# Performance work log

Measured on AMD Instinct MI355X. Metric: run time of the kernel, lower is better.

The kernel has to match this reference:

```python
import jax, jax.numpy as jnp
import numpy as np

N_NODES = 50000
N_EDGES = 800000
IN_DIM = 128
HIDDEN = 128


def setup_inputs() -> dict:
    key = jax.random.key(0)
    ks = jax.random.split(key, 6)
    x = jax.random.normal(ks[0], (N_NODES, IN_DIM), dtype=jnp.float32)
    edge_index = jax.random.randint(ks[1], (2, N_EDGES), 0, N_NODES, dtype=jnp.int32)
    W1 = jax.random.normal(ks[2], (IN_DIM, HIDDEN), dtype=jnp.float32) * 0.05
    b1 = jnp.zeros((HIDDEN,), dtype=jnp.float32)
    W2 = jax.random.normal(ks[3], (HIDDEN, HIDDEN), dtype=jnp.float32) * 0.05
    b2 = jnp.zeros((HIDDEN,), dtype=jnp.float32)
    return {"x": x, "edge_index": edge_index, "W1": W1, "b1": b1, "W2": W2, "b2": b2}


def _gcn_conv(x, W, b, src, dst, norm, n):
    # PyG GCNConv: linear transform, then normalized sum-aggregate, then bias.
    h = x @ W                                  # [N, H]
    msg = h[src] * norm[:, None]               # gather + scale  [E+N, H]
    out = jax.ops.segment_sum(msg, dst, num_segments=n)
    return out + b


def reference(x, edge_index, W1, b1, W2, b2):
    n = x.shape[0]
    # add self-loops (GCNConv default add_self_loops=True)
    loops = jnp.arange(n, dtype=edge_index.dtype)
    src = jnp.concatenate([edge_index[0], loops])
    dst = jnp.concatenate([edge_index[1], loops])
    # symmetric normalization: deg over destination nodes (edge_weight = 1)
    deg = jax.ops.segment_sum(jnp.ones(src.shape, dtype=x.dtype), dst, num_segments=n)
    dinv = jax.lax.rsqrt(deg)                  # deg >= 1 because of self-loops
    norm = dinv[src] * dinv[dst]               # [E+N]
    h = jax.nn.relu(_gcn_conv(x, W1, b1, src, dst, norm, n))
    return _gcn_conv(h, W2, b2, src, dst, norm, n)
```

## Files before the change

kernel.cpp:

```cpp
#include <hip/hip_runtime.h>

#define N_NODES 50000
#define N_EDGES 800000
#define DIM 128
#define CHUNK 4096
#define GRID 196
#define SEG_CAP 6144
#define GEMM_BLOCKS 391
#define GA 196
#define GB (GEMM_BLOCKS - GA)

typedef __attribute__((ext_vector_type(8))) short bf16x8;
typedef __attribute__((ext_vector_type(4))) float f32x4;


__device__ inline unsigned rne_bf16(float f) {
    unsigned u = __float_as_uint(f);
    return (u + 0x7FFFu + ((u >> 16) & 1u)) >> 16;
}
__device__ inline unsigned pk_bf16(float a, float b) {
    return rne_bf16(a) | (rne_bf16(b) << 16);
}
__device__ inline float bf_lo(unsigned u) { return __uint_as_float(u << 16); }
__device__ inline float bf_hi(unsigned u) { return __uint_as_float(u & 0xFFFF0000u); }


__device__ void fragw_build(const float* __restrict__ W, uint4* __restrict__ fh,
                            uint4* __restrict__ fl, int slot) {
    const int lane = slot & 63, tile = slot >> 6;
    const int c = tile >> 2, q = tile & 3;
    const int k0 = q * 32 + ((lane >> 4) << 3);
    const int col = c * 16 + (lane & 15);
    unsigned h[8], l[8];
#pragma unroll
    for (int j = 0; j < 8; ++j) {
        float w = W[(size_t)(k0 + j) * DIM + col];
        unsigned hb = rne_bf16(w);
        h[j] = hb;
        l[j] = rne_bf16(w - __uint_as_float(hb << 16));
    }
    uint4 uh, ul;
    uh.x = h[0] | (h[1] << 16); uh.y = h[2] | (h[3] << 16);
    uh.z = h[4] | (h[5] << 16); uh.w = h[6] | (h[7] << 16);
    ul.x = l[0] | (l[1] << 16); ul.y = l[2] | (l[3] << 16);
    ul.z = l[4] | (l[5] << 16); ul.w = l[6] | (l[7] << 16);
    fh[slot] = uh;
    fl[slot] = ul;
}


__global__ __launch_bounds__(256) void chunk_hist_fragw(const int* __restrict__ dst,
                                                        int* __restrict__ chist,
                                                        const float* __restrict__ W1,
                                                        const float* __restrict__ W2,
                                                        uint4* f1h, uint4* f1l,
                                                        uint4* f2h, uint4* f2l) {
    const int bid = blockIdx.x;
    if (bid < GRID) {
        __shared__ int hist[256];
        const int t = threadIdx.x;
        const int eb = bid * CHUNK;
        const int cnt = min(CHUNK, N_EDGES - eb);
        hist[t] = 0;
        __syncthreads();
        for (int i = t; i < cnt; i += 256)
            atomicAdd(&hist[dst[eb + i] >> 8], 1);
        __syncthreads();
        chist[bid * 256 + t] = hist[t];
    } else {
        const int b2 = bid - GRID;
        const int slot = (b2 & 7) * 256 + threadIdx.x;
        if (b2 < 8) fragw_build(W1, f1h, f1l, slot);
        else        fragw_build(W2, f2h, f2l, slot);
    }
}


__device__ void gemm_body(const float* __restrict__ X,
                          const uint4* __restrict__ fWh,
                          const uint4* __restrict__ fWl,
                          uint2* __restrict__ O, int gb, char* smem) {
    const int t = threadIdx.x;

    {
        uint4* s4 = (uint4*)smem;
        for (int i = t; i < 2048; i += 256) {
            s4[i] = fWh[i];
            s4[2048 + i] = fWl[i];
        }
    }
    __syncthreads();

    const int w = t >> 6, lane = t & 63;
    const int lrow = lane & 15, lgrp = lane >> 4;
    const int rbase = gb * 128;

    bf16x8 Ah[2][4], Al[2][4];
#pragma unroll
    for (int m = 0; m < 2; ++m) {
        const int r = rbase + w * 32 + m * 16 + lrow;
        const bool ok = (r < N_NODES);
        const float4* xp = (const float4*)(X + (size_t)r * DIM + lgrp * 8);
#pragma unroll
        for (int q = 0; q < 4; ++q) {
            float4 a0 = ok ? xp[q * 8]     : make_float4(0.f, 0.f, 0.f, 0.f);
            float4 a1 = ok ? xp[q * 8 + 1] : make_float4(0.f, 0.f, 0.f, 0.f);
            float f[8] = {a0.x, a0.y, a0.z, a0.w, a1.x, a1.y, a1.z, a1.w};
            bf16x8 hi, lo;
#pragma unroll
            for (int j = 0; j < 8; ++j) {
                unsigned hb = rne_bf16(f[j]);
                hi[j] = (short)hb;
                lo[j] = (short)rne_bf16(f[j] - __uint_as_float(hb << 16));
            }
            Ah[m][q] = hi;
            Al[m][q] = lo;
        }
    }

    f32x4 acc[2][8];
#pragma unroll
    for (int m = 0; m < 2; ++m)
#pragma unroll
        for (int c = 0; c < 8; ++c)
            acc[m][c] = (f32x4){0.f, 0.f, 0.f, 0.f};

    const bf16x8* Bh = (const bf16x8*)smem;
    const bf16x8* Bl = (const bf16x8*)(smem + 32768);
#pragma unroll
    for (int c = 0; c < 8; ++c) {
#pragma unroll
        for (int q = 0; q < 4; ++q) {
            bf16x8 bh = Bh[(c * 4 + q) * 64 + lane];
            bf16x8 bl = Bl[(c * 4 + q) * 64 + lane];
#pragma unroll
            for (int m = 0; m < 2; ++m) {
                acc[m][c] = __builtin_amdgcn_mfma_f32_16x16x32_bf16(Ah[m][q], bh, acc[m][c], 0, 0, 0);
                acc[m][c] = __builtin_amdgcn_mfma_f32_16x16x32_bf16(Al[m][q], bh, acc[m][c], 0, 0, 0);
                acc[m][c] = __builtin_amdgcn_mfma_f32_16x16x32_bf16(Ah[m][q], bl, acc[m][c], 0, 0, 0);
            }
        }
    }

    __syncthreads();
    float* Lf = (float*)smem;
#pragma unroll
    for (int m = 0; m < 2; ++m)
#pragma unroll
        for (int c = 0; c < 8; ++c)
#pragma unroll
            for (int rg = 0; rg < 4; ++rg)
                Lf[(w * 32 + m * 16 + lgrp * 4 + rg) * DIM + c * 16 + lrow] = acc[m][c][rg];
    __syncthreads();

    const float4* Lf4 = (const float4*)smem;
    for (int idx = t; idx < 4096; idx += 256) {
        const int row = idx >> 5, s = idx & 31;
        const int gr = rbase + row;
        if (gr < N_NODES) {
            float4 v = Lf4[idx];
            uint2 o;
            o.x = pk_bf16(v.x, v.y);
            o.y = pk_bf16(v.z, v.w);
            O[(size_t)gr * 32 + s] = o;
        }
    }
}


__device__ void sort_scatter_body(const int* __restrict__ src,
                                  const int* __restrict__ dst,
                                  const int* __restrict__ chist,
                                  unsigned* __restrict__ sorted,
                                  int* __restrict__ bbase_g,
                                  int bid, char* smem) {
    int* hist  = (int*)smem;
    int* sc    = hist + 256;
    int* lbase = sc + 256;
    int* lcur  = lbase + 256;
    int* gbase = lcur + 256;
    unsigned* sl = (unsigned*)(smem + 5 * 1024);

    const int t = threadIdx.x;
    const int eb = bid * CHUNK;
    const int cnt = min(CHUNK, N_EDGES - eb);

    int sum = 0, myoff = 0;
    for (int c = 0; c < GRID; ++c) {
        int v = chist[c * 256 + t];
        if (c == bid) myoff = sum;
        sum += v;
    }
    hist[t] = chist[bid * 256 + t];
    sc[t] = sum;
    __syncthreads();
    for (int off = 1; off < 256; off <<= 1) {
        int u = (t >= off) ? sc[t - off] : 0;
        __syncthreads();
        sc[t] += u;
        __syncthreads();
    }
    gbase[t] = (sc[t] - sum) + myoff;
    if (bid == 0) bbase_g[t] = sc[t] - sum;
    __syncthreads();

    sc[t] = hist[t];
    __syncthreads();
    for (int off = 1; off < 256; off <<= 1) {
        int u = (t >= off) ? sc[t - off] : 0;
        __syncthreads();
        sc[t] += u;
        __syncthreads();
    }
    int ex = sc[t] - hist[t];
    lbase[t] = ex;
    lcur[t] = ex;
    __syncthreads();

    for (int i = t; i < cnt; i += 256) {
        int s = src[eb + i], d = dst[eb + i];
        int b = d >> 8;
        int p = atomicAdd(&lcur[b], 1);
        sl[p] = ((unsigned)b << 24) | ((unsigned)(d & 255) << 16) | (unsigned)s;
    }
    __syncthreads();
    for (int i = t; i < cnt; i += 256) {
        unsigned rec = sl[i];
        int b = rec >> 24;
        sorted[gbase[b] + (i - lbase[b])] = rec;
    }
}


__device__ void csr_build_body(const unsigned* __restrict__ sorted,
                               const int* __restrict__ bbase,
                               int* __restrict__ rowptr,
                               float* __restrict__ dinv,
                               int* __restrict__ csr,
                               int k, char* smem) {
    int* hist = (int*)smem;
    int* sc   = hist + 256;
    int* lcur = sc + 256;
    int* seg  = (int*)(smem + 3 * 1024);

    const int t = threadIdx.x;
    const int base = bbase[k];
    const int cntk = ((k == 255) ? N_EDGES : bbase[k + 1]) - base;
    if (k == 0 && t == 0) rowptr[N_NODES] = N_EDGES;

    hist[t] = 0;
    __syncthreads();
    for (int i = t; i < cntk; i += 256)
        atomicAdd(&hist[(sorted[base + i] >> 16) & 255], 1);
    __syncthreads();

    const int node = (k << 8) + t;
    const int dv = hist[t];
    if (node < N_NODES) dinv[node] = rsqrtf((float)dv + 1.0f);

    sc[t] = dv;
    __syncthreads();
    for (int off = 1; off < 256; off <<= 1) {
        int u = (t >= off) ? sc[t - off] : 0;
        __syncthreads();
        sc[t] += u;
        __syncthreads();
    }
    int ex = sc[t] - dv;
    if (node < N_NODES) rowptr[node] = base + ex;
    lcur[t] = ex;
    __syncthreads();

    if (cntk <= SEG_CAP) {
        for (int i = t; i < cntk; i += 256) {
            unsigned rec = sorted[base + i];
            int p = atomicAdd(&lcur[(rec >> 16) & 255], 1);
            seg[p] = (int)(rec & 0xFFFFu);
        }
        __syncthreads();
        for (int i = t; i < cntk; i += 256)
            csr[base + i] = seg[i];
    } else {
        for (int i = t; i < cntk; i += 256) {
            unsigned rec = sorted[base + i];
            int p = atomicAdd(&lcur[(rec >> 16) & 255], 1);
            csr[base + p] = (int)(rec & 0xFFFFu);
        }
    }
}


__global__ __launch_bounds__(256, 2) void sort_gemm(const int* __restrict__ src,
                                                    const int* __restrict__ dst,
                                                    const int* __restrict__ chist,
                                                    unsigned* __restrict__ sorted,
                                                    int* __restrict__ bbase_g,
                                                    const float* __restrict__ X,
                                                    const uint4* __restrict__ fWh,
                                                    const uint4* __restrict__ fWl,
                                                    uint2* __restrict__ O) {
    __shared__ __align__(16) char smem[65536];
    if (blockIdx.x < GRID)
        sort_scatter_body(src, dst, chist, sorted, bbase_g, blockIdx.x, smem);
    else
        gemm_body(X, fWh, fWl, O, blockIdx.x - GRID, smem);
}

__global__ __launch_bounds__(256, 2) void csr_gemm(const unsigned* __restrict__ sorted,
                                                   const int* __restrict__ bbase,
                                                   int* __restrict__ rowptr,
                                                   float* __restrict__ dinv,
                                                   int* __restrict__ csr,
                                                   const float* __restrict__ X,
                                                   const uint4* __restrict__ fWh,
                                                   const uint4* __restrict__ fWl,
                                                   uint2* __restrict__ O) {
    __shared__ __align__(16) char smem[65536];
    if (blockIdx.x < GRID)
        csr_build_body(sorted, bbase, rowptr, dinv, csr, blockIdx.x, smem);
    else
        gemm_body(X, fWh, fWl, O, blockIdx.x - GRID + GA, smem);
}


__device__ inline float4 agg_node(int node, const uint2* __restrict__ H2,
                                  const int* __restrict__ rowptr,
                                  const int* __restrict__ csr,
                                  const float* __restrict__ dinv,
                                  const float4* __restrict__ b4, int relu) {
    const int lane = threadIdx.x & 63;
    const int half = lane >> 5;
    const int col  = lane & 31;

    const float dn = dinv[node];
    float4 acc = make_float4(0.f, 0.f, 0.f, 0.f);
    if (half == 0) {
        uint2 v = H2[(size_t)node * 32 + col];
        acc.x = dn * bf_lo(v.x); acc.y = dn * bf_hi(v.x);
        acc.z = dn * bf_lo(v.y); acc.w = dn * bf_hi(v.y);
    }

    int j = rowptr[node];
    const int end = rowptr[node + 1];

#define ACC(v, ds) do { \
        acc.x = fmaf((ds), bf_lo((v).x), acc.x); \
        acc.y = fmaf((ds), bf_hi((v).x), acc.y); \
        acc.z = fmaf((ds), bf_lo((v).y), acc.z); \
        acc.w = fmaf((ds), bf_hi((v).y), acc.w); } while (0)

    for (; j + 16 <= end; j += 16) {
        int s0 = csr[j +  0 + half], s1 = csr[j +  2 + half];
        int s2 = csr[j +  4 + half], s3 = csr[j +  6 + half];
        int s4 = csr[j +  8 + half], s5 = csr[j + 10 + half];
        int s6 = csr[j + 12 + half], s7 = csr[j + 14 + half];
        uint2 v0 = H2[(size_t)s0 * 32 + col]; float d0 = dinv[s0];
        uint2 v1 = H2[(size_t)s1 * 32 + col]; float d1 = dinv[s1];
        uint2 v2 = H2[(size_t)s2 * 32 + col]; float d2 = dinv[s2];
        uint2 v3 = H2[(size_t)s3 * 32 + col]; float d3 = dinv[s3];
        uint2 v4 = H2[(size_t)s4 * 32 + col]; float d4 = dinv[s4];
        uint2 v5 = H2[(size_t)s5 * 32 + col]; float d5 = dinv[s5];
        uint2 v6 = H2[(size_t)s6 * 32 + col]; float d6 = dinv[s6];
        uint2 v7 = H2[(size_t)s7 * 32 + col]; float d7 = dinv[s7];
        ACC(v0, d0); ACC(v1, d1); ACC(v2, d2); ACC(v3, d3);
        ACC(v4, d4); ACC(v5, d5); ACC(v6, d6); ACC(v7, d7);
    }
    if (j + 8 <= end) {
        int s0 = csr[j + half], s1 = csr[j + 2 + half];
        int s2 = csr[j + 4 + half], s3 = csr[j + 6 + half];
        uint2 v0 = H2[(size_t)s0 * 32 + col]; float d0 = dinv[s0];
        uint2 v1 = H2[(size_t)s1 * 32 + col]; float d1 = dinv[s1];
        uint2 v2 = H2[(size_t)s2 * 32 + col]; float d2 = dinv[s2];
        uint2 v3 = H2[(size_t)s3 * 32 + col]; float d3 = dinv[s3];
        ACC(v0, d0); ACC(v1, d1); ACC(v2, d2); ACC(v3, d3);
        j += 8;
    }
    if (j + 4 <= end) {
        int s0 = csr[j + half], s1 = csr[j + 2 + half];
        uint2 v0 = H2[(size_t)s0 * 32 + col]; float d0 = dinv[s0];
        uint2 v1 = H2[(size_t)s1 * 32 + col]; float d1 = dinv[s1];
        ACC(v0, d0); ACC(v1, d1);
        j += 4;
    }
    if (j + 2 <= end) {
        int s = csr[j + half];
        uint2 v = H2[(size_t)s * 32 + col]; float d0 = dinv[s];
        ACC(v, d0);
        j += 2;
    }
    if (j < end && half == 0) {
        int s = csr[j];
        uint2 v = H2[(size_t)s * 32 + col]; float d0 = dinv[s];
        ACC(v, d0);
    }
#undef ACC

    acc.x += __shfl_xor(acc.x, 32, 64);
    acc.y += __shfl_xor(acc.y, 32, 64);
    acc.z += __shfl_xor(acc.z, 32, 64);
    acc.w += __shfl_xor(acc.w, 32, 64);

    float4 o = make_float4(0.f, 0.f, 0.f, 0.f);
    if (half == 0) {
        float4 bb = b4[col];
        o.x = acc.x * dn + bb.x;
        o.y = acc.y * dn + bb.y;
        o.z = acc.z * dn + bb.z;
        o.w = acc.w * dn + bb.w;
        if (relu) {
            o.x = fmaxf(o.x, 0.f); o.y = fmaxf(o.y, 0.f);
            o.z = fmaxf(o.z, 0.f); o.w = fmaxf(o.w, 0.f);
        }
    }
    return o;
}


__global__ __launch_bounds__(256) void aggregate_kernel(const uint2* __restrict__ H2,
                                                        const int* __restrict__ rowptr,
                                                        const int* __restrict__ csr,
                                                        const float* __restrict__ dinv,
                                                        const float4* __restrict__ b4,
                                                        float4* __restrict__ out,
                                                        int relu) {
    int node = blockIdx.x * 4 + (threadIdx.x >> 6);
    if (node >= N_NODES) return;
    float4 o = agg_node(node, H2, rowptr, csr, dinv, b4, relu);
    const int lane = threadIdx.x & 63;
    if (lane < 32) out[(size_t)node * 32 + lane] = o;
}


__global__ __launch_bounds__(512, 2) void agg_gemm2(const uint2* __restrict__ H2,
                                                    const int* __restrict__ rowptr,
                                                    const int* __restrict__ csr,
                                                    const float* __restrict__ dinv,
                                                    const float4* __restrict__ b4,
                                                    const uint4* __restrict__ fWh,
                                                    const uint4* __restrict__ fWl,
                                                    uint2* __restrict__ O) {
    __shared__ __align__(16) char smem[65536];
    uint2* Hh = (uint2*)smem;
    uint2* Hl = (uint2*)(smem + 32768);
    const int t = threadIdx.x;
    const int w = t >> 6;
    const int lane = t & 63;
    const int half = lane >> 5;
    const int g = lane & 31;
    const int rbase = blockIdx.x * 128;

    for (int i = 0; i < 16; ++i) {
        const int row = w * 16 + i;
        const int node = rbase + row;
        float4 o = make_float4(0.f, 0.f, 0.f, 0.f);
        if (node < N_NODES)
            o = agg_node(node, H2, rowptr, csr, dinv, b4, 1);
        if (half == 0) {
            unsigned hx = rne_bf16(o.x), hy = rne_bf16(o.y);
            unsigned hz = rne_bf16(o.z), hw = rne_bf16(o.w);
            unsigned lx = rne_bf16(o.x - __uint_as_float(hx << 16));
            unsigned ly = rne_bf16(o.y - __uint_as_float(hy << 16));
            unsigned lz = rne_bf16(o.z - __uint_as_float(hz << 16));
            unsigned lw = rne_bf16(o.w - __uint_as_float(hw << 16));
            const int idx = row * 32 + (((g >> 1) ^ (row & 7)) << 1) + (g & 1);
            uint2 hv; hv.x = hx | (hy << 16); hv.y = hz | (hw << 16);
            uint2 lv; lv.x = lx | (ly << 16); lv.y = lz | (lw << 16);
            Hh[idx] = hv;
            Hl[idx] = lv;
        }
    }
    __syncthreads();

    const int lrow = lane & 15, lgrp = lane >> 4;
    const int arow = w * 16 + lrow;
    f32x4 acc[8];
#pragma unroll
    for (int c = 0; c < 8; ++c) acc[c] = (f32x4){0.f, 0.f, 0.f, 0.f};

#pragma unroll
    for (int q = 0; q < 4; ++q) {
        const int idx = arow * 32 + ((((q << 2) + lgrp) ^ (arow & 7)) << 1);
        bf16x8 Ah = *(const bf16x8*)&Hh[idx];
        bf16x8 Al = *(const bf16x8*)&Hl[idx];
#pragma unroll
        for (int c = 0; c < 8; ++c) {
            bf16x8 bh = *(const bf16x8*)&fWh[(c * 4 + q) * 64 + lane];
            bf16x8 bl = *(const bf16x8*)&fWl[(c * 4 + q) * 64 + lane];
            acc[c] = __builtin_amdgcn_mfma_f32_16x16x32_bf16(Ah, bh, acc[c], 0, 0, 0);
            acc[c] = __builtin_amdgcn_mfma_f32_16x16x32_bf16(Al, bh, acc[c], 0, 0, 0);
            acc[c] = __builtin_amdgcn_mfma_f32_16x16x32_bf16(Ah, bl, acc[c], 0, 0, 0);
        }
    }
    __syncthreads();

    float* Lf = (float*)smem;
#pragma unroll
    for (int c = 0; c < 8; ++c)
#pragma unroll
        for (int rg = 0; rg < 4; ++rg)
            Lf[(w * 16 + lgrp * 4 + rg) * DIM + c * 16 + lrow] = acc[c][rg];
    __syncthreads();

    const float4* Lf4 = (const float4*)smem;
    for (int idx = t; idx < 4096; idx += 512) {
        const int row = idx >> 5, s = idx & 31;
        const int gr = rbase + row;
        if (gr < N_NODES) {
            float4 v = Lf4[idx];
            uint2 o2;
            o2.x = pk_bf16(v.x, v.y);
            o2.y = pk_bf16(v.z, v.w);
            O[(size_t)gr * 32 + s] = o2;
        }
    }
}


extern "C" void kernel_launch(void* const* d_in, const int* in_sizes, int n_in,
                              void* d_out, int out_size, void* d_ws, size_t ws_size,
                              hipStream_t stream) {
    const float* x  = (const float*)d_in[0];
    const int*   ei = (const int*)d_in[1];
    const float* W1 = (const float*)d_in[2];
    const float* b1 = (const float*)d_in[3];
    const float* W2 = (const float*)d_in[4];
    const float* b2 = (const float*)d_in[5];
    float* out = (float*)d_out;

    const int* src = ei;
    const int* dst = ei + N_EDGES;

    char* p = (char*)d_ws;
    int*      chist  = (int*)p;              p += GRID * 256 * 4;
    float*    dinv   = (float*)p;            p += ((N_NODES * 4 + 1023) & ~1023);
    int*      rowptr = (int*)p;              p += (((N_NODES + 1) * 4 + 1023) & ~1023);
    unsigned* sorted = (unsigned*)p;         p += ((N_EDGES * 4 + 1023) & ~1023);
    int*      csr    = (int*)p;              p += ((N_EDGES * 4 + 1023) & ~1023);
    int*      bbase  = (int*)p;              p += 1024;
    uint4*    f1h    = (uint4*)p;            p += 32768;
    uint4*    f1l    = (uint4*)p;            p += 32768;
    uint4*    f2h    = (uint4*)p;            p += 32768;
    uint4*    f2l    = (uint4*)p;            p += 32768;
    uint2*    hp     = (uint2*)p;            p += (size_t)N_NODES * DIM * 2;
    uint2*    hp2    = (uint2*)p;

    const int aggBlocks = (N_NODES + 3) / 4;

    chunk_hist_fragw<<<GRID + 16, 256, 0, stream>>>(dst, chist, W1, W2,
                                                    f1h, f1l, f2h, f2l);
    sort_gemm<<<GRID + GA, 256, 0, stream>>>(src, dst, chist, sorted, bbase,
                                             x, f1h, f1l, hp);
    csr_gemm<<<GRID + GB, 256, 0, stream>>>(sorted, bbase, rowptr, dinv, csr,
                                            x, f1h, f1l, hp);

    agg_gemm2<<<GEMM_BLOCKS, 512, 0, stream>>>(hp, rowptr, csr, dinv,
                                               (const float4*)b1, f2h, f2l, hp2);

    aggregate_kernel<<<aggBlocks, 256, 0, stream>>>(hp2, rowptr, csr, dinv,
                                                    (const float4*)b2, (float4*)out, 0);
}
```

Before: 228.5 us.

## Split fused layer-1 aggregate+GEMM into separate aggregate and GEMM kernels

Replaces the fused agg_gemm2 kernel, which had 391 large blocks doing the irregular layer-1 aggregation serially per wave, with a fine-grained aggregate_h1 kernel that writes hi/lo bf16 splits of h1 to global memory. A separate gemm_xw2 kernel then loads W2 fragments into LDS and computes two 16-row tiles per wave, reusing each B fragment. The aim is better parallelism and latency hiding for the gather-heavy aggregation. The cost is an extra launch and a 25.6 MB round trip of h1 (hi+lo) through global memory.

```diff
diff --git a/kernel.cpp b/kernel.cpp
--- a/kernel.cpp
+++ b/kernel.cpp
@@ -416,101 +416,127 @@
 }
 
 
-__global__ __launch_bounds__(256) void aggregate_kernel(const uint2* __restrict__ H2,
-                                                        const int* __restrict__ rowptr,
-                                                        const int* __restrict__ csr,
-                                                        const float* __restrict__ dinv,
-                                                        const float4* __restrict__ b4,
-                                                        float4* __restrict__ out,
-                                                        int relu) {
-    int node = blockIdx.x * 4 + (threadIdx.x >> 6);
-    if (node >= N_NODES) return;
-    float4 o = agg_node(node, H2, rowptr, csr, dinv, b4, relu);
-    const int lane = threadIdx.x & 63;
-    if (lane < 32) out[(size_t)node * 32 + lane] = o;
-}
-
-
-__global__ __launch_bounds__(512, 2) void agg_gemm2(const uint2* __restrict__ H2,
+__global__ __launch_bounds__(256) void aggregate_h1(const uint2* __restrict__ H2,
                                                     const int* __restrict__ rowptr,
                                                     const int* __restrict__ csr,
                                                     const float* __restrict__ dinv,
                                                     const float4* __restrict__ b4,
-                                                    const uint4* __restrict__ fWh,
-                                                    const uint4* __restrict__ fWl,
-                                                    uint2* __restrict__ O) {
+                                                    uint2* __restrict__ h1h,
+                                                    uint2* __restrict__ h1l) {
+    int node = blockIdx.x * 4 + (threadIdx.x >> 6);
+    if (node >= N_NODES) return;
+    float4 o = agg_node(node, H2, rowptr, csr, dinv, b4, 1);
+    const int lane = threadIdx.x & 63;
+    if (lane < 32) {
+        unsigned hx = rne_bf16(o.x), hy = rne_bf16(o.y);
+        unsigned hz = rne_bf16(o.z), hw = rne_bf16(o.w);
+        unsigned lx = rne_bf16(o.x - __uint_as_float(hx << 16));
+        unsigned ly = rne_bf16(o.y - __uint_as_float(hy << 16));
+        unsigned lz = rne_bf16(o.z - __uint_as_float(hz << 16));
+        unsigned lw = rne_bf16(o.w - __uint_as_float(hw << 16));
+        uint2 hv; hv.x = hx | (hy << 16); hv.y = hz | (hw << 16);
+        uint2 lv; lv.x = lx | (ly << 16); lv.y = lz | (lw << 16);
+        h1h[(size_t)node * 32 + lane] = hv;
+        h1l[(size_t)node * 32 + lane] = lv;
+    }
+}
+
+
+__global__ __launch_bounds__(256) void aggregate_out(const uint2* __restrict__ H2,
+                                                     const int* __restrict__ rowptr,
+                                                     const int* __restrict__ csr,
+                                                     const float* __restrict__ dinv,
+                                                     const float4* __restrict__ b4,
+                                                     float4* __restrict__ out) {
+    int node = blockIdx.x * 4 + (threadIdx.x >> 6);
+    if (node >= N_NODES) return;
+    float4 o = agg_node(node, H2, rowptr, csr, dinv, b4, 0);
+    const int lane = threadIdx.x & 63;
+    if (lane < 32) out[(size_t)node * 32 + lane] = o;
+}
+
+
+__global__ __launch_bounds__(256, 2) void gemm_xw2(const uint2* __restrict__ h1h,
+                                                   const uint2* __restrict__ h1l,
+                                                   const uint4* __restrict__ fWh,
+                                                   const uint4* __restrict__ fWl,
+                                                   uint2* __restrict__ O) {
     __shared__ __align__(16) char smem[65536];
-    uint2* Hh = (uint2*)smem;
-    uint2* Hl = (uint2*)(smem + 32768);
     const int t = threadIdx.x;
-    const int w = t >> 6;
-    const int lane = t & 63;
-    const int half = lane >> 5;
-    const int g = lane & 31;
+
+    {
+        uint4* s4 = (uint4*)smem;
+        for (int i = t; i < 2048; i += 256) {
+            s4[i] = fWh[i];
+            s4[2048 + i] = fWl[i];
+        }
+    }
+    __syncthreads();
+
+    const int w = t >> 6, lane = t & 63;
+    const int lrow = lane & 15, lgrp = lane >> 4;
     const int rbase = blockIdx.x * 128;
 
-    for (int i = 0; i < 16; ++i) {
-        const int row = w * 16 + i;
-        const int node = rbase + row;
-        float4 o = make_float4(0.f, 0.f, 0.f, 0.f);
-        if (node < N_NODES)
-            o = agg_node(node, H2, rowptr, csr, dinv, b4, 1);
-        if (half == 0) {
-            unsigned hx = rne_bf16(o.x), hy = rne_bf16(o.y);
-            unsigned hz = rne_bf16(o.z), hw = rne_bf16(o.w);
-            unsigned lx = rne_bf16(o.x - __uint_as_float(hx << 16));
-            unsigned ly = rne_bf16(o.y - __uint_as_float(hy << 16));
-            unsigned lz = rne_bf16(o.z - __uint_as_float(hz << 16));
-            unsigned lw = rne_bf16(o.w - __uint_as_float(hw << 16));
-            const int idx = row * 32 + (((g >> 1) ^ (row & 7)) << 1) + (g & 1);
-            uint2 hv; hv.x = hx | (hy << 16); hv.y = hz | (hw << 16);
-            uint2 lv; lv.x = lx | (ly << 16); lv.y = lz | (lw << 16);
-            Hh[idx] = hv;
-            Hl[idx] = lv;
-        }
-    }
-    __syncthreads();
-
-    const int lrow = lane & 15, lgrp = lane >> 4;
-    const int arow = w * 16 + lrow;
-    f32x4 acc[8];
-#pragma unroll
-    for (int c = 0; c < 8; ++c) acc[c] = (f32x4){0.f, 0.f, 0.f, 0.f};
-
-#pragma unroll
-    for (int q = 0; q < 4; ++q) {
-        const int idx = arow * 32 + ((((q << 2) + lgrp) ^ (arow & 7)) << 1);
-        bf16x8 Ah = *(const bf16x8*)&Hh[idx];
-        bf16x8 Al = *(const bf16x8*)&Hl[idx];
-#pragma unroll
-        for (int c = 0; c < 8; ++c) {
-            bf16x8 bh = *(const bf16x8*)&fWh[(c * 4 + q) * 64 + lane];
-            bf16x8 bl = *(const bf16x8*)&fWl[(c * 4 + q) * 64 + lane];
-            acc[c] = __builtin_amdgcn_mfma_f32_16x16x32_bf16(Ah, bh, acc[c], 0, 0, 0);
-            acc[c] = __builtin_amdgcn_mfma_f32_16x16x32_bf16(Al, bh, acc[c], 0, 0, 0);
-            acc[c] = __builtin_amdgcn_mfma_f32_16x16x32_bf16(Ah, bl, acc[c], 0, 0, 0);
-        }
-    }
-    __syncthreads();
-
+    bf16x8 Ah[2][4], Al[2][4];
+    const bf16x8 zz = (bf16x8){0,0,0,0,0,0,0,0};
+#pragma unroll
+    for (int m = 0; m < 2; ++m) {
+        const int r = rbase + w * 32 + m * 16 + lrow;
+        const bool ok = (r < N_NODES);
+        const uint2* ph = h1h + (size_t)r * 32 + lgrp * 2;
+        const uint2* pl = h1l + (size_t)r * 32 + lgrp * 2;
+#pragma unroll
+        for (int q = 0; q < 4; ++q) {
+            Ah[m][q] = ok ? *(const bf16x8*)(ph + q * 8) : zz;
+            Al[m][q] = ok ? *(const bf16x8*)(pl + q * 8) : zz;
+        }
+    }
+
+    f32x4 acc[2][8];
+#pragma unroll
+    for (int m = 0; m < 2; ++m)
+#pragma unroll
+        for (int c = 0; c < 8; ++c)
+            acc[m][c] = (f32x4){0.f, 0.f, 0.f, 0.f};
+
+    const bf16x8* Bh = (const bf16x8*)smem;
+    const bf16x8* Bl = (const bf16x8*)(smem + 32768);
+#pragma unroll
+    for (int c = 0; c < 8; ++c) {
+#pragma unroll
+        for (int q = 0; q < 4; ++q) {
+            bf16x8 bh = Bh[(c * 4 + q) * 64 + lane];
+            bf16x8 bl = Bl[(c * 4 + q) * 64 + lane];
+#pragma unroll
+            for (int m = 0; m < 2; ++m) {
+                acc[m][c] = __builtin_amdgcn_mfma_f32_16x16x32_bf16(Ah[m][q], bh, acc[m][c], 0, 0, 0);
+                acc[m][c] = __builtin_amdgcn_mfma_f32_16x16x32_bf16(Al[m][q], bh, acc[m][c], 0, 0, 0);
+                acc[m][c] = __builtin_amdgcn_mfma_f32_16x16x32_bf16(Ah[m][q], bl, acc[m][c], 0, 0, 0);
+            }
+        }
+    }
+
+    __syncthreads();
     float* Lf = (float*)smem;
 #pragma unroll
-    for (int c = 0; c < 8; ++c)
-#pragma unroll
-        for (int rg = 0; rg < 4; ++rg)
-            Lf[(w * 16 + lgrp * 4 + rg) * DIM + c * 16 + lrow] = acc[c][rg];
+    for (int m = 0; m < 2; ++m)
+#pragma unroll
+        for (int c = 0; c < 8; ++c)
+#pragma unroll
+            for (int rg = 0; rg < 4; ++rg)
+                Lf[(w * 32 + m * 16 + lgrp * 4 + rg) * DIM + c * 16 + lrow] = acc[m][c][rg];
     __syncthreads();
 
     const float4* Lf4 = (const float4*)smem;
-    for (int idx = t; idx < 4096; idx += 512) {
+    for (int idx = t; idx < 4096; idx += 256) {
         const int row = idx >> 5, s = idx & 31;
         const int gr = rbase + row;
         if (gr < N_NODES) {
             float4 v = Lf4[idx];
-            uint2 o2;
-            o2.x = pk_bf16(v.x, v.y);
-            o2.y = pk_bf16(v.z, v.w);
-            O[(size_t)gr * 32 + s] = o2;
+            uint2 o;
+            o.x = pk_bf16(v.x, v.y);
+            o.y = pk_bf16(v.z, v.w);
+            O[(size_t)gr * 32 + s] = o;
         }
     }
 }
@@ -542,6 +568,8 @@
     uint4*    f2h    = (uint4*)p;            p += 32768;
     uint4*    f2l    = (uint4*)p;            p += 32768;
     uint2*    hp     = (uint2*)p;            p += (size_t)N_NODES * DIM * 2;
+    uint2*    h1h    = (uint2*)p;            p += (size_t)N_NODES * DIM * 2;
+    uint2*    h1l    = (uint2*)p;            p += (size_t)N_NODES * DIM * 2;
     uint2*    hp2    = (uint2*)p;
 
     const int aggBlocks = (N_NODES + 3) / 4;
@@ -553,9 +581,11 @@
     csr_gemm<<<GRID + GB, 256, 0, stream>>>(sorted, bbase, rowptr, dinv, csr,
                                             x, f1h, f1l, hp);
 
-    agg_gemm2<<<GEMM_BLOCKS, 512, 0, stream>>>(hp, rowptr, csr, dinv,
-                                               (const float4*)b1, f2h, f2l, hp2);
-
-    aggregate_kernel<<<aggBlocks, 256, 0, stream>>>(hp2, rowptr, csr, dinv,
-                                                    (const float4*)b2, (float4*)out, 0);
-}
+    aggregate_h1<<<aggBlocks, 256, 0, stream>>>(hp, rowptr, csr, dinv,
+                                                (const float4*)b1, h1h, h1l);
+
+    gemm_xw2<<<GEMM_BLOCKS, 256, 0, stream>>>(h1h, h1l, f2h, f2l, hp2);
+
+    aggregate_out<<<aggBlocks, 256, 0, stream>>>(hp2, rowptr, csr, dinv,
+                                                 (const float4*)b2, (float4*)out);
+}
```

After: 210.9 us. 7.7% less time.
